# Optimization experiments

Hardware: AMD Instinct MI355X
Metric: run time of the kernel (lower is better)

## Reference

```python
import jax, jax.numpy as jnp
import numpy as np

B, S, H2 = 32, 4096, 512  # H2 = 2*hidden_size


def setup_inputs() -> dict:
    key = jax.random.key(0)
    ks = jax.random.split(key, 10)
    s = 1.0 / np.sqrt(H2)
    return {
        "decoder_state": jax.random.normal(ks[0], (B, 1, H2), jnp.float32),
        "encoder_outputs": jax.random.normal(ks[1], (B, S, H2), jnp.float32),
        "coverage_vector": jax.random.uniform(ks[2], (B, S, H2), jnp.float32),
        "W_h": jax.random.uniform(ks[3], (H2, H2), jnp.float32, -s, s),
        "b_h": jax.random.uniform(ks[4], (H2,), jnp.float32, -s, s),
        "W_s": jax.random.uniform(ks[5], (H2, H2), jnp.float32, -s, s),
        "b_s": jax.random.uniform(ks[6], (H2,), jnp.float32, -s, s),
        "W_c": jax.random.uniform(ks[7], (H2, H2), jnp.float32, -s, s),
        "b_c": jax.random.uniform(ks[8], (H2,), jnp.float32, -s, s),
        "v": jax.random.uniform(ks[9], (H2, 1), jnp.float32, -s, s),
    }


def reference(decoder_state, encoder_outputs, coverage_vector,
              W_h, b_h, W_s, b_s, W_c, b_c, v):
    # additive attention features: [B, S, 2H]
    e = jnp.tanh(encoder_outputs @ W_h + b_h
                 + decoder_state @ W_s + b_s      # broadcasts over S
                 + coverage_vector @ W_c + b_c)
    scores = e @ v                                # [B, S, 1]
    attn_dist = jax.nn.softmax(scores, axis=1)    # softmax over source positions
    # weighted sum of encoder outputs: [B, 1, 2H]
    h_star_t = jnp.einsum('bsi,bsd->bid', attn_dist, encoder_outputs)
    coverage_new = coverage_vector + attn_dist    # broadcast over feature dim
    return h_star_t, attn_dist, coverage_new
```

## Files before the change

kernel.cpp:

```cpp
#include <hip/hip_runtime.h>
#include <hip/hip_bf16.h>
#include <stdint.h>

#define H2    512
#define BATCH 32
#define SEQ   4096
#define BM    128
#define BK    64
#define NKT   16

typedef __attribute__((ext_vector_type(4))) float f32x4;
typedef __attribute__((ext_vector_type(8))) short bf16x8;

typedef __attribute__((address_space(3))) unsigned int       as3_uint;
typedef const __attribute__((address_space(1))) unsigned int as1_uint;

__device__ __forceinline__ unsigned short f2bf(float f) {
    union { float f; unsigned u; } v; v.f = f;
    unsigned r = v.u + 0x7FFF + ((v.u >> 16) & 1);
    return (unsigned short)(r >> 16);
}

__device__ __forceinline__ float fast_tanh(float x) {
    float e = __builtin_amdgcn_exp2f(x * 2.88539008177793f);
    return 1.0f - 2.0f * __builtin_amdgcn_rcpf(e + 1.0f);
}

__global__ void kprep_w(const float* __restrict__ Wh, const float* __restrict__ Wc,
                        unsigned short* __restrict__ wt) {
    int c   = blockIdx.x * blockDim.x + threadIdx.x;
    int col = c & 511;
    int kk8 = (c >> 9) & 7;
    int kt  = c >> 12;
    int kbase = kt * 64 + kk8 * 8;
    unsigned short tmp[8];
#pragma unroll
    for (int j = 0; j < 8; ++j) {
        int kg = kbase + j;
        float w = (kg < 512) ? Wh[kg * 512 + col] : Wc[(kg - 512) * 512 + col];
        tmp[j] = f2bf(w);
    }
    unsigned byteoff = (unsigned)(col * 128 + kk8 * 16) ^ ((unsigned)(col & 7) << 4);
    unsigned short* dst = wt + (size_t)kt * (512 * 64) + byteoff / 2;
    *reinterpret_cast<uint4*>(dst) = *reinterpret_cast<const uint4*>(tmp);
}

__global__ void kprep_q(const float* __restrict__ dec, const float* __restrict__ Ws,
                        const float* __restrict__ bh, const float* __restrict__ bs,
                        const float* __restrict__ bc, float* __restrict__ q) {
    __shared__ float dsh[512];
    int b = blockIdx.x, t = threadIdx.x;
    dsh[t]       = dec[b * 512 + t];
    dsh[t + 256] = dec[b * 512 + 256 + t];
    __syncthreads();
    float a0 = 0.f, a1 = 0.f;
#pragma unroll 4
    for (int k = 0; k < 512; ++k) {
        float d = dsh[k];
        a0 = fmaf(d, Ws[k * 512 + t], a0);
        a1 = fmaf(d, Ws[k * 512 + 256 + t], a1);
    }
    q[b * 512 + t]       = a0 + bh[t] + bs[t] + bc[t];
    q[b * 512 + 256 + t] = a1 + bh[256 + t] + bs[256 + t] + bc[256 + t];
}

__launch_bounds__(512, 2)
__global__ void kgemm(const float* __restrict__ enc, const float* __restrict__ cov,
                      const unsigned short* __restrict__ wt,
                      const float* __restrict__ q, const float* __restrict__ vvec,
                      float* __restrict__ scores) {
    __shared__ unsigned short Asm[BM * BK];
    __shared__ unsigned short Bsm[H2 * BK];
    __shared__ float qv[H2];
    __shared__ float vv[H2];
    __shared__ float sred[BM][4];

    int tid  = threadIdx.x;
    int wid  = tid >> 6, lane = tid & 63;
    int wm   = wid >> 2, wn = wid & 3;

    int bidx = blockIdx.x;
    int cpx  = gridDim.x >> 3;
    int swz  = (bidx & 7) * cpx + (bidx >> 3);

    int row0 = swz * BM;
    const float* encb = enc + (size_t)row0 * H2;
    const float* covb = cov + (size_t)row0 * H2;

    if (tid < 512) { qv[tid] = q[(row0 >> 12) * 512 + tid]; vv[tid] = vvec[tid]; }

    f32x4 acc[4][8] = {};

    int arow = tid >> 2;
    int kq   = (tid & 3) * 16;
    unsigned awb0 = ((unsigned)(arow * 128 + kq * 2))      ^ ((unsigned)(arow & 7) << 4);
    unsigned awb1 = ((unsigned)(arow * 128 + kq * 2 + 16)) ^ ((unsigned)(arow & 7) << 4);

    for (int kt = 0; kt < NKT; ++kt) {
        {
            const float* src = (kt < 8) ? (encb + (size_t)arow * H2 + kt * 64 + kq)
                                        : (covb + (size_t)arow * H2 + (kt - 8) * 64 + kq);
            float fv[16];
            *reinterpret_cast<f32x4*>(fv)      = *reinterpret_cast<const f32x4*>(src);
            *reinterpret_cast<f32x4*>(fv + 4)  = *reinterpret_cast<const f32x4*>(src + 4);
            *reinterpret_cast<f32x4*>(fv + 8)  = *reinterpret_cast<const f32x4*>(src + 8);
            *reinterpret_cast<f32x4*>(fv + 12) = *reinterpret_cast<const f32x4*>(src + 12);
            unsigned short hv[16];
#pragma unroll
            for (int j = 0; j < 16; ++j) hv[j] = f2bf(fv[j]);
            *reinterpret_cast<uint4*>((char*)Asm + awb0) = *reinterpret_cast<const uint4*>(hv);
            *reinterpret_cast<uint4*>((char*)Asm + awb1) = *reinterpret_cast<const uint4*>(hv + 8);
        }
        {
            const unsigned short* gt = wt + (size_t)kt * (512 * 64) + wid * 4096 + lane * 8;
#pragma unroll
            for (int i = 0; i < 8; ++i) {
                __builtin_amdgcn_global_load_lds((as1_uint*)(gt + i * 512),
                                                 (as3_uint*)(Bsm + wid * 4096 + i * 512),
                                                 16, 0, 0);
            }
        }
        __syncthreads();
#pragma unroll
        for (int ks = 0; ks < 2; ++ks) {
            bf16x8 af[4], bfr[8];
#pragma unroll
            for (int mi = 0; mi < 4; ++mi) {
                int row = wm * 64 + mi * 16 + (lane & 15);
                unsigned bo = ((unsigned)(row * 128 + ks * 64 + (lane >> 4) * 16))
                              ^ ((unsigned)(row & 7) << 4);
                af[mi] = *reinterpret_cast<const bf16x8*>((const char*)Asm + bo);
            }
#pragma unroll
            for (int ni = 0; ni < 8; ++ni) {
                int col = wn * 128 + ni * 16 + (lane & 15);
                unsigned bo = ((unsigned)(col * 128 + ks * 64 + (lane >> 4) * 16))
                              ^ ((unsigned)(col & 7) << 4);
                bfr[ni] = *reinterpret_cast<const bf16x8*>((const char*)Bsm + bo);
            }
#pragma unroll
            for (int mi = 0; mi < 4; ++mi)
#pragma unroll
                for (int ni = 0; ni < 8; ++ni)
                    acc[mi][ni] = __builtin_amdgcn_mfma_f32_16x16x32_bf16(
                        af[mi], bfr[ni], acc[mi][ni], 0, 0, 0);
        }
        __syncthreads();
    }

    float ps[4][4] = {};
#pragma unroll
    for (int mi = 0; mi < 4; ++mi)
#pragma unroll
        for (int ni = 0; ni < 8; ++ni) {
            int colg = wn * 128 + ni * 16 + (lane & 15);
            float qq = qv[colg], vl = vv[colg];
#pragma unroll
            for (int j = 0; j < 4; ++j) {
                float e = fast_tanh(acc[mi][ni][j] + qq);
                ps[mi][j] = fmaf(e, vl, ps[mi][j]);
            }
        }
#pragma unroll
    for (int mi = 0; mi < 4; ++mi)
#pragma unroll
        for (int j = 0; j < 4; ++j) {
            float s = ps[mi][j];
            s += __shfl_xor(s, 1);
            s += __shfl_xor(s, 2);
            s += __shfl_xor(s, 4);
            s += __shfl_xor(s, 8);
            if ((lane & 15) == 0)
                sred[wm * 64 + mi * 16 + (lane >> 4) * 4 + j][wn] = s;
        }
    __syncthreads();
    if (tid < BM) {
        float s = sred[tid][0] + sred[tid][1] + sred[tid][2] + sred[tid][3];
        scores[row0 + tid] = s;
    }
}

__global__ void ksoftmax(const float* __restrict__ scores, float* __restrict__ out) {
    __shared__ float redm[16];
    __shared__ float reds[16];
    int b = blockIdx.x, t = threadIdx.x, lane = t & 63, w = t >> 6;
    if (t < 512) out[b * 512 + t] = 0.0f;
    f32x4 sv = *reinterpret_cast<const f32x4*>(scores + b * 4096 + t * 4);
    float m = fmaxf(fmaxf(sv[0], sv[1]), fmaxf(sv[2], sv[3]));
#pragma unroll
    for (int o = 1; o < 64; o <<= 1) m = fmaxf(m, __shfl_xor(m, o));
    if (lane == 0) redm[w] = m;
    __syncthreads();
    float mm = redm[0];
#pragma unroll
    for (int i = 1; i < 16; ++i) mm = fmaxf(mm, redm[i]);

    f32x4 p;
#pragma unroll
    for (int j = 0; j < 4; ++j)
        p[j] = __builtin_amdgcn_exp2f((sv[j] - mm) * 1.4426950408889634f);
    float s = p[0] + p[1] + p[2] + p[3];
#pragma unroll
    for (int o = 1; o < 64; o <<= 1) s += __shfl_xor(s, o);
    if (lane == 0) reds[w] = s;
    __syncthreads();
    float tot = 0.f;
#pragma unroll
    for (int i = 0; i < 16; ++i) tot += reds[i];
    float rinv = __builtin_amdgcn_rcpf(tot);
    p *= rinv;
    *reinterpret_cast<f32x4*>(out + 16384 + b * 4096 + t * 4) = p;
}

__global__ void kcov(const float* __restrict__ enc, const float* __restrict__ cov,
                     float* __restrict__ out) {
    const float* attn = out + 16384;
    float* covn  = out + 16384 + 131072;
    float* hstar = out;
    int blk = blockIdx.x;
    int b = blk >> 6, ck = blk & 63;
    int s0 = ck * 64;
    int t  = threadIdx.x;
    int f4 = (t & 127) * 4;
    int rp = t >> 7;
    size_t base = (size_t)b * SEQ * H2;
    f32x4 h = {0.f, 0.f, 0.f, 0.f};
#pragma unroll 2
    for (int i = 0; i < 32; ++i) {
        int s = s0 + i * 2 + rp;
        float a = attn[b * 4096 + s];
        size_t idx = base + (size_t)s * H2 + f4;
        f32x4 e4 = *reinterpret_cast<const f32x4*>(enc + idx);
        f32x4 c4 = *reinterpret_cast<const f32x4*>(cov + idx);
        c4 += a;
        __builtin_nontemporal_store(c4, reinterpret_cast<f32x4*>(covn + idx));
        h += a * e4;
    }
    int off = b * 512 + f4;
    atomicAdd(&hstar[off + 0], h[0]);
    atomicAdd(&hstar[off + 1], h[1]);
    atomicAdd(&hstar[off + 2], h[2]);
    atomicAdd(&hstar[off + 3], h[3]);
}

extern "C" void kernel_launch(void* const* d_in, const int* in_sizes, int n_in,
                              void* d_out, int out_size, void* d_ws, size_t ws_size,
                              hipStream_t stream) {
    const float* dec = (const float*)d_in[0];
    const float* enc = (const float*)d_in[1];
    const float* cov = (const float*)d_in[2];
    const float* Wh  = (const float*)d_in[3];
    const float* bh  = (const float*)d_in[4];
    const float* Ws  = (const float*)d_in[5];
    const float* bs  = (const float*)d_in[6];
    const float* Wc  = (const float*)d_in[7];
    const float* bc  = (const float*)d_in[8];
    const float* v   = (const float*)d_in[9];
    float* out = (float*)d_out;

    char* ws = (char*)d_ws;
    unsigned short* wt = (unsigned short*)ws;
    float* q      = (float*)(ws + (1 << 20));
    float* scores = (float*)(ws + (1 << 20) + 65536);

    kprep_w <<<dim3(256),  dim3(256),  0, stream>>>(Wh, Wc, wt);
    kprep_q <<<dim3(32),   dim3(256),  0, stream>>>(dec, Ws, bh, bs, bc, q);
    kgemm   <<<dim3(1024), dim3(512),  0, stream>>>(enc, cov, wt, q, v, scores);
    ksoftmax<<<dim3(32),   dim3(1024), 0, stream>>>(scores, out);
    kcov    <<<dim3(2048), dim3(256),  0, stream>>>(enc, cov, out);
}
```

Baseline: 436.0 us.

## Load weight fragments straight to registers and double-buffer a smaller A tile

The weight matrix is now prepacked in MFMA fragment order, so each wave loads its B fragments directly from global memory (L2-resident) into registers instead of staging a 64 KB tile through LDS. The A tile shrinks to 64 rows and is double-buffered in LDS, with the next tile's fp32 loads issued before the MFMAs and converted and stored afterwards, leaving one barrier per k-step. With far less LDS and 8 waves each owning a 64-column slice, occupancy rises (launch bounds 4) and the grid doubles. The tradeoff is more total global/L2 traffic for weights, since each block now rereads the whole weight matrix for half as many rows.

```diff
diff --git a/kernel.cpp b/kernel.cpp
--- a/kernel.cpp
+++ b/kernel.cpp
@@ -5,15 +5,12 @@
 #define H2    512
 #define BATCH 32
 #define SEQ   4096
-#define BM    128
+#define BM    64
 #define BK    64
 #define NKT   16
 
 typedef __attribute__((ext_vector_type(4))) float f32x4;
 typedef __attribute__((ext_vector_type(8))) short bf16x8;
-
-typedef __attribute__((address_space(3))) unsigned int       as3_uint;
-typedef const __attribute__((address_space(1))) unsigned int as1_uint;
 
 __device__ __forceinline__ unsigned short f2bf(float f) {
     union { float f; unsigned u; } v; v.f = f;
@@ -28,21 +25,21 @@
 
 __global__ void kprep_w(const float* __restrict__ Wh, const float* __restrict__ Wc,
                         unsigned short* __restrict__ wt) {
-    int c   = blockIdx.x * blockDim.x + threadIdx.x;
-    int col = c & 511;
-    int kk8 = (c >> 9) & 7;
-    int kt  = c >> 12;
-    int kbase = kt * 64 + kk8 * 8;
+    int c    = blockIdx.x * blockDim.x + threadIdx.x;
+    int lane = c & 63;
+    int cb   = (c >> 6) & 31;
+    int ks   = (c >> 11) & 1;
+    int kt   = c >> 12;
+    int col  = cb * 16 + (lane & 15);
+    int k0   = kt * 64 + ks * 32 + (lane >> 4) * 8;
     unsigned short tmp[8];
 #pragma unroll
     for (int j = 0; j < 8; ++j) {
-        int kg = kbase + j;
+        int kg = k0 + j;
         float w = (kg < 512) ? Wh[kg * 512 + col] : Wc[(kg - 512) * 512 + col];
         tmp[j] = f2bf(w);
     }
-    unsigned byteoff = (unsigned)(col * 128 + kk8 * 16) ^ ((unsigned)(col & 7) << 4);
-    unsigned short* dst = wt + (size_t)kt * (512 * 64) + byteoff / 2;
-    *reinterpret_cast<uint4*>(dst) = *reinterpret_cast<const uint4*>(tmp);
+    *reinterpret_cast<uint4*>(wt + (size_t)c * 8) = *reinterpret_cast<const uint4*>(tmp);
 }
 
 __global__ void kprep_q(const float* __restrict__ dec, const float* __restrict__ Ws,
@@ -64,96 +61,94 @@
     q[b * 512 + 256 + t] = a1 + bh[256 + t] + bs[256 + t] + bc[256 + t];
 }
 
-__launch_bounds__(512, 2)
+__launch_bounds__(512, 4)
 __global__ void kgemm(const float* __restrict__ enc, const float* __restrict__ cov,
                       const unsigned short* __restrict__ wt,
                       const float* __restrict__ q, const float* __restrict__ vvec,
                       float* __restrict__ scores) {
-    __shared__ unsigned short Asm[BM * BK];
-    __shared__ unsigned short Bsm[H2 * BK];
+    __shared__ unsigned short Asm[2][BM * BK];
     __shared__ float qv[H2];
     __shared__ float vv[H2];
-    __shared__ float sred[BM][4];
+    __shared__ float sred[BM][8];
 
     int tid  = threadIdx.x;
-    int wid  = tid >> 6, lane = tid & 63;
-    int wm   = wid >> 2, wn = wid & 3;
-
-    int bidx = blockIdx.x;
+    int lane = tid & 63, wn = tid >> 6;
+
     int cpx  = gridDim.x >> 3;
-    int swz  = (bidx & 7) * cpx + (bidx >> 3);
-
+    int swz  = (blockIdx.x & 7) * cpx + (blockIdx.x >> 3);
     int row0 = swz * BM;
-    const float* encb = enc + (size_t)row0 * H2;
-    const float* covb = cov + (size_t)row0 * H2;
-
-    if (tid < 512) { qv[tid] = q[(row0 >> 12) * 512 + tid]; vv[tid] = vvec[tid]; }
-
-    f32x4 acc[4][8] = {};
-
-    int arow = tid >> 2;
-    int kq   = (tid & 3) * 16;
-    unsigned awb0 = ((unsigned)(arow * 128 + kq * 2))      ^ ((unsigned)(arow & 7) << 4);
-    unsigned awb1 = ((unsigned)(arow * 128 + kq * 2 + 16)) ^ ((unsigned)(arow & 7) << 4);
+
+    qv[tid] = q[(row0 >> 12) * H2 + tid];
+    vv[tid] = vvec[tid];
+
+    int r = tid >> 3, k8 = tid & 7;
+    const float* ae = enc + (size_t)(row0 + r) * H2 + k8 * 8;
+    const float* ac = cov + (size_t)(row0 + r) * H2 + k8 * 8;
+    unsigned awb = (unsigned)(r * 128 + ((k8 * 16) ^ ((r & 7) << 4)));
+
+    unsigned arb0 = (unsigned)((lane & 15) * 128 +
+                    ((((lane >> 4) << 4))      ^ ((lane & 7) << 4)));
+    unsigned arb1 = (unsigned)((lane & 15) * 128 +
+                    (((64 + ((lane >> 4) << 4))) ^ ((lane & 7) << 4)));
+
+    f32x4 acc[4][4] = {};
+
+    {
+        f32x4 a0 = *reinterpret_cast<const f32x4*>(ae);
+        f32x4 a1 = *reinterpret_cast<const f32x4*>(ae + 4);
+        union { unsigned short h[8]; uint4 u; } t;
+#pragma unroll
+        for (int j = 0; j < 4; ++j) { t.h[j] = f2bf(a0[j]); t.h[4 + j] = f2bf(a1[j]); }
+        *reinterpret_cast<uint4*>((char*)Asm[0] + awb) = t.u;
+    }
+    __syncthreads();
 
     for (int kt = 0; kt < NKT; ++kt) {
-        {
-            const float* src = (kt < 8) ? (encb + (size_t)arow * H2 + kt * 64 + kq)
-                                        : (covb + (size_t)arow * H2 + (kt - 8) * 64 + kq);
-            float fv[16];
-            *reinterpret_cast<f32x4*>(fv)      = *reinterpret_cast<const f32x4*>(src);
-            *reinterpret_cast<f32x4*>(fv + 4)  = *reinterpret_cast<const f32x4*>(src + 4);
-            *reinterpret_cast<f32x4*>(fv + 8)  = *reinterpret_cast<const f32x4*>(src + 8);
-            *reinterpret_cast<f32x4*>(fv + 12) = *reinterpret_cast<const f32x4*>(src + 12);
-            unsigned short hv[16];
-#pragma unroll
-            for (int j = 0; j < 16; ++j) hv[j] = f2bf(fv[j]);
-            *reinterpret_cast<uint4*>((char*)Asm + awb0) = *reinterpret_cast<const uint4*>(hv);
-            *reinterpret_cast<uint4*>((char*)Asm + awb1) = *reinterpret_cast<const uint4*>(hv + 8);
-        }
-        {
-            const unsigned short* gt = wt + (size_t)kt * (512 * 64) + wid * 4096 + lane * 8;
-#pragma unroll
-            for (int i = 0; i < 8; ++i) {
-                __builtin_amdgcn_global_load_lds((as1_uint*)(gt + i * 512),
-                                                 (as3_uint*)(Bsm + wid * 4096 + i * 512),
-                                                 16, 0, 0);
-            }
+        int cur = kt & 1;
+        bf16x8 bfr[2][4];
+        const bf16x8* bp0 = reinterpret_cast<const bf16x8*>(wt) +
+                            ((size_t)(kt * 2 + 0) * 32 + wn * 4) * 64 + lane;
+        const bf16x8* bp1 = reinterpret_cast<const bf16x8*>(wt) +
+                            ((size_t)(kt * 2 + 1) * 32 + wn * 4) * 64 + lane;
+#pragma unroll
+        for (int ni = 0; ni < 4; ++ni) bfr[0][ni] = bp0[ni * 64];
+#pragma unroll
+        for (int ni = 0; ni < 4; ++ni) bfr[1][ni] = bp1[ni * 64];
+        f32x4 p0, p1;
+        if (kt + 1 < NKT) {
+            const float* src = (kt + 1 < 8) ? (ae + (kt + 1) * 64) : (ac + (kt - 7) * 64);
+            p0 = *reinterpret_cast<const f32x4*>(src);
+            p1 = *reinterpret_cast<const f32x4*>(src + 4);
+        }
+#pragma unroll
+        for (int ks = 0; ks < 2; ++ks) {
+            bf16x8 af[4];
+#pragma unroll
+            for (int mi = 0; mi < 4; ++mi)
+                af[mi] = *reinterpret_cast<const bf16x8*>(
+                    (const char*)Asm[cur] + mi * 2048 + (ks ? arb1 : arb0));
+#pragma unroll
+            for (int mi = 0; mi < 4; ++mi)
+#pragma unroll
+                for (int ni = 0; ni < 4; ++ni)
+                    acc[mi][ni] = __builtin_amdgcn_mfma_f32_16x16x32_bf16(
+                        af[mi], bfr[ks][ni], acc[mi][ni], 0, 0, 0);
+        }
+        if (kt + 1 < NKT) {
+            union { unsigned short h[8]; uint4 u; } t;
+#pragma unroll
+            for (int j = 0; j < 4; ++j) { t.h[j] = f2bf(p0[j]); t.h[4 + j] = f2bf(p1[j]); }
+            *reinterpret_cast<uint4*>((char*)Asm[cur ^ 1] + awb) = t.u;
         }
         __syncthreads();
-#pragma unroll
-        for (int ks = 0; ks < 2; ++ks) {
-            bf16x8 af[4], bfr[8];
-#pragma unroll
-            for (int mi = 0; mi < 4; ++mi) {
-                int row = wm * 64 + mi * 16 + (lane & 15);
-                unsigned bo = ((unsigned)(row * 128 + ks * 64 + (lane >> 4) * 16))
-                              ^ ((unsigned)(row & 7) << 4);
-                af[mi] = *reinterpret_cast<const bf16x8*>((const char*)Asm + bo);
-            }
-#pragma unroll
-            for (int ni = 0; ni < 8; ++ni) {
-                int col = wn * 128 + ni * 16 + (lane & 15);
-                unsigned bo = ((unsigned)(col * 128 + ks * 64 + (lane >> 4) * 16))
-                              ^ ((unsigned)(col & 7) << 4);
-                bfr[ni] = *reinterpret_cast<const bf16x8*>((const char*)Bsm + bo);
-            }
-#pragma unroll
-            for (int mi = 0; mi < 4; ++mi)
-#pragma unroll
-                for (int ni = 0; ni < 8; ++ni)
-                    acc[mi][ni] = __builtin_amdgcn_mfma_f32_16x16x32_bf16(
-                        af[mi], bfr[ni], acc[mi][ni], 0, 0, 0);
-        }
-        __syncthreads();
     }
 
     float ps[4][4] = {};
 #pragma unroll
     for (int mi = 0; mi < 4; ++mi)
 #pragma unroll
-        for (int ni = 0; ni < 8; ++ni) {
-            int colg = wn * 128 + ni * 16 + (lane & 15);
+        for (int ni = 0; ni < 4; ++ni) {
+            int colg = wn * 64 + ni * 16 + (lane & 15);
             float qq = qv[colg], vl = vv[colg];
 #pragma unroll
             for (int j = 0; j < 4; ++j) {
@@ -171,11 +166,13 @@
             s += __shfl_xor(s, 4);
             s += __shfl_xor(s, 8);
             if ((lane & 15) == 0)
-                sred[wm * 64 + mi * 16 + (lane >> 4) * 4 + j][wn] = s;
+                sred[mi * 16 + (lane >> 4) * 4 + j][wn] = s;
         }
     __syncthreads();
     if (tid < BM) {
-        float s = sred[tid][0] + sred[tid][1] + sred[tid][2] + sred[tid][3];
+        float s = 0.f;
+#pragma unroll
+        for (int w = 0; w < 8; ++w) s += sred[tid][w];
         scores[row0 + tid] = s;
     }
 }
@@ -265,7 +262,7 @@
 
     kprep_w <<<dim3(256),  dim3(256),  0, stream>>>(Wh, Wc, wt);
     kprep_q <<<dim3(32),   dim3(256),  0, stream>>>(dec, Ws, bh, bs, bc, q);
-    kgemm   <<<dim3(1024), dim3(512),  0, stream>>>(enc, cov, wt, q, v, scores);
+    kgemm   <<<dim3(2048), dim3(512),  0, stream>>>(enc, cov, wt, q, v, scores);
     ksoftmax<<<dim3(32),   dim3(1024), 0, stream>>>(scores, out);
     kcov    <<<dim3(2048), dim3(256),  0, stream>>>(enc, cov, out);
 }
```

After: 401.5 us. 1.09x faster.
